# Optimization experiments

Measured on AMD Instinct MI355X. Metric: run time of the kernel, lower is better.

The kernel has to match this reference:

```python
import jax, jax.numpy as jnp
import numpy as np
from jax import lax

K = 3  # kernel size
CO = 64  # out_channels
CI = 64  # in_channels


def setup_inputs() -> dict:
    key = jax.random.key(0)
    k1, k2, k3, k4, k5 = jax.random.split(key, 5)
    x = jax.random.normal(k1, (16, CI, 128, 128), dtype=jnp.float32)
    w1 = jax.random.normal(k2, (2 * CI, 32), dtype=jnp.float32) * 0.05
    b1 = jax.random.normal(k3, (32,), dtype=jnp.float32) * 0.05
    w2 = jax.random.normal(k4, (32, CO * CI * K * K), dtype=jnp.float32) * 0.05
    b2 = jax.random.normal(k5, (CO * CI * K * K,), dtype=jnp.float32) * 0.05
    return {"x": x, "w1": w1, "b1": b1, "w2": w2, "b2": b2}


def reference(x, w1, b1, w2, b2):
    B = x.shape[0]
    # per-sample channel statistics over spatial dims (torch.std is unbiased, ddof=1)
    mean = jnp.mean(x, axis=(2, 3))                      # [B, CI]
    std = jnp.std(x, axis=(2, 3), ddof=1)                # [B, CI]
    stats = jnp.concatenate([mean, std], axis=-1)        # [B, 2*CI]
    h = jax.nn.relu(stats @ w1 + b1)                     # [B, 32]
    kernels = (h @ w2 + b2).reshape(B, CO, CI, K, K)     # per-sample conv kernels

    def conv_one(xi, wi):
        # xi: [CI,H,W], wi: [CO,CI,K,K]; stride=1, padding=1, no bias
        return lax.conv_general_dilated(
            xi[None], wi, window_strides=(1, 1), padding=[(1, 1), (1, 1)],
            dimension_numbers=("NCHW", "OIHW", "NCHW"))[0]

    return jax.vmap(conv_one)(x, kernels)                # [B, CO, H, W]
```

## Files before the change

### kernel.cpp

```cpp
#include <hip/hip_runtime.h>
#include <hip/hip_bf16.h>


#define B_ 16
#define NPIX 16384
#define KEL 36864
#define XT_RS 8320

typedef __attribute__((ext_vector_type(4))) float f32x4;
typedef __attribute__((ext_vector_type(8))) short short8;

static __device__ __forceinline__ short bf16_of(float f) {
    __hip_bfloat16 h = __float2bfloat16(f);
    return *reinterpret_cast<short*>(&h);
}

__global__ __launch_bounds__(256) void xpose_stats(const float* __restrict__ x,
                                                   short* __restrict__ xT,
                                                   float* __restrict__ part) {
    int b = blockIdx.x, cig = blockIdx.y, pt = blockIdx.z;
    int t = threadIdx.x;
    int y = pt * 8 + (t >> 5);
    int x0 = (t & 31) * 4;

    const float* xb = x + ((size_t)(b * 64 + cig * 8)) * NPIX;
    short* xTb = xT + (size_t)b * 128 * XT_RS;

    float s[8], ss[8];
    f32x4 v[8];
    #pragma unroll
    for (int c = 0; c < 8; c++) {
        v[c] = *(const f32x4*)(xb + (size_t)c * NPIX + y * 128 + x0);
        s[c]  = v[c][0] + v[c][1] + v[c][2] + v[c][3];
        ss[c] = v[c][0]*v[c][0] + v[c][1]*v[c][1] + v[c][2]*v[c][2] + v[c][3]*v[c][3];
    }
    #pragma unroll
    for (int xi = 0; xi < 4; xi++) {
        short8 o;
        #pragma unroll
        for (int c = 0; c < 8; c++) o[c] = bf16_of(v[c][xi]);
        *(short8*)(xTb + ((size_t)(y * 130 + x0 + xi + 1)) * 64 + cig * 8) = o;
    }
    if (t < 16) {
        int y2 = pt * 8 + (t & 7);
        int col = (t & 8) ? 129 : 0;
        short8 z = {0, 0, 0, 0, 0, 0, 0, 0};
        *(short8*)(xTb + ((size_t)(y2 * 130 + col)) * 64 + cig * 8) = z;
    }

    __shared__ float red[4][16];
    int lane = t & 63, w = t >> 6;
    #pragma unroll
    for (int c = 0; c < 8; c++) {
        float a = s[c], q = ss[c];
        for (int off = 32; off; off >>= 1) { a += __shfl_down(a, off); q += __shfl_down(q, off); }
        if (lane == 0) { red[w][c * 2] = a; red[w][c * 2 + 1] = q; }
    }
    __syncthreads();
    if (t < 16)
        part[((size_t)((b * 8 + cig) * 16 + pt)) * 16 + t] =
            red[0][t] + red[1][t] + red[2][t] + red[3][t];
}

__global__ __launch_bounds__(256) void kern_gen(const float* __restrict__ part,
                                                const float* __restrict__ w1,
                                                const float* __restrict__ b1,
                                                const float* __restrict__ w2,
                                                const float* __restrict__ b2,
                                                short* __restrict__ wT) {
    __shared__ float st[16][128];
    __shared__ float hT[32][16];
    int t = threadIdx.x;

    for (int id = t; id < 1024; id += 256) {
        int b = id >> 6, ci = id & 63;
        const float* pb = part + ((size_t)((b * 8 + (ci >> 3)) * 16)) * 16 + (ci & 7) * 2;
        float s = 0.f, q = 0.f;
        #pragma unroll
        for (int p = 0; p < 16; p++) { s += pb[p * 16]; q += pb[p * 16 + 1]; }
        float mean = s * (1.f / NPIX);
        float var = fmaxf((q - s * mean) * (1.f / (NPIX - 1)), 0.f);
        st[b][ci] = mean;
        st[b][64 + ci] = sqrtf(var);
    }
    __syncthreads();
    for (int id = t; id < 512; id += 256) {
        int b = id >> 5, jj = id & 31;
        float acc = b1[jj];
        for (int i = 0; i < 128; i++) acc += st[b][i] * w1[i * 32 + jj];
        hT[jj][b] = fmaxf(acc, 0.f);
    }
    __syncthreads();

    int j = blockIdx.x * 128 + (t & 127);
    int bh = t >> 7;
    float wv[32];
    #pragma unroll
    for (int i = 0; i < 32; i++) wv[i] = w2[(size_t)i * KEL + j];
    float bv = b2[j];

    float acc[8];
    #pragma unroll
    for (int k = 0; k < 8; k++) acc[k] = bv;
    #pragma unroll
    for (int i = 0; i < 32; i++) {
        float wvi = wv[i];
        const f32x4* hr = (const f32x4*)&hT[i][bh * 8];
        #pragma unroll
        for (int q4 = 0; q4 < 2; q4++) {
            f32x4 hq = hr[q4];
            acc[q4 * 4 + 0] += hq[0] * wvi;
            acc[q4 * 4 + 1] += hq[1] * wvi;
            acc[q4 * 4 + 2] += hq[2] * wvi;
            acc[q4 * 4 + 3] += hq[3] * wvi;
        }
    }

    int co = j / 576;
    int rem = j - co * 576;
    int ci = rem / 9;
    int tap = rem - ci * 9;
    size_t dst = (size_t)tap * 4096 + co * 64 + ((((ci >> 3) ^ (co & 7)) << 3) | (ci & 7));
    #pragma unroll
    for (int k = 0; k < 8; k++)
        wT[(size_t)(bh * 8 + k) * KEL + dst] = bf16_of(acc[k]);
}

__global__ __launch_bounds__(256, 2) void conv_mfma(const short* __restrict__ xT,
                                                    const short* __restrict__ wT,
                                                    float* __restrict__ out) {
    __shared__ __align__(16) short xls[10 * 272 * 8];
    __shared__ __align__(16) short wls[9 * 256 * 8];

    int b = blockIdx.x;
    int xt = blockIdx.y & 3, cog = blockIdx.y >> 2;
    int ys = blockIdx.z;
    int x0 = xt * 32, y0 = ys * 8;
    int t = threadIdx.x;
    int l = t & 63, w = t >> 6;
    int xq = w & 1, rh = w >> 1;
    int l15 = l & 15, lg = l >> 4;

    const short* xTb = xT + (size_t)b * 128 * XT_RS;
    const short* wTb = wT + (size_t)b * KEL + cog * 2048;

    #pragma unroll
    for (int it = 0; it < 9; it++) {
        __builtin_amdgcn_global_load_lds(
            (const __attribute__((address_space(1))) void*)(wTb + (size_t)it * 4096 + t * 8),
            (__attribute__((address_space(3))) void*)(wls + (it * 256 + (t & ~63)) * 8),
            16, 0, 0);
    }
    #pragma unroll
    for (int lr = 0; lr < 10; lr++) {
        int y = y0 - 1 + lr;
        if (y < 0 || y > 127) {
            short8 z8 = {0, 0, 0, 0, 0, 0, 0, 0};
            #pragma unroll
            for (int it = 0; it < 2; it++) {
                int e = it * 256 + t;
                if (e < 272) *(short8*)(xls + (lr * 272 + e) * 8) = z8;
            }
        } else {
            #pragma unroll
            for (int it = 0; it < 2; it++) {
                int e = it * 256 + t;
                if (e < 272) {
                    int xi = e >> 3, s = e & 7;
                    const short* src = xTb + (size_t)y * XT_RS
                        + (x0 + xi) * 64 + ((s ^ (xi & 7)) << 3);
                    __builtin_amdgcn_global_load_lds(
                        (const __attribute__((address_space(1))) void*)src,
                        (__attribute__((address_space(3))) void*)
                            (xls + (lr * 272 + it * 256 + (t & ~63)) * 8),
                        16, 0, 0);
                }
            }
        }
    }
    asm volatile("s_waitcnt vmcnt(0)" ::: "memory");
    __syncthreads();

    f32x4 acc[2][4];
    #pragma unroll
    for (int f = 0; f < 2; f++)
        #pragma unroll
        for (int r = 0; r < 4; r++) acc[f][r] = (f32x4){0.f, 0.f, 0.f, 0.f};

    #pragma unroll
    for (int kp = 0; kp < 2; kp++) {
        int sig = kp * 4 + lg;
        int pa = sig ^ (l15 & 7);
        #pragma unroll
        for (int tap = 0; tap < 9; tap++) {
            const int dy = tap / 3, dx = tap % 3;
            short8 a0 = *(const short8*)&wls[(tap * 256 + l15 * 8 + pa) * 8];
            short8 a1 = *(const short8*)&wls[(tap * 256 + (16 + l15) * 8 + pa) * 8];
            int xi = xq * 16 + l15 + dx;
            int sw = sig ^ (xi & 7);
            #pragma unroll
            for (int r = 0; r < 4; r++) {
                int row = rh * 4 + r + dy;
                short8 bf = *(const short8*)&xls[(row * 272 + xi * 8 + sw) * 8];
                acc[0][r] = __builtin_amdgcn_mfma_f32_16x16x32_bf16(a0, bf, acc[0][r], 0, 0, 0);
                acc[1][r] = __builtin_amdgcn_mfma_f32_16x16x32_bf16(a1, bf, acc[1][r], 0, 0, 0);
            }
        }
    }

    #pragma unroll
    for (int f = 0; f < 2; f++) {
        #pragma unroll
        for (int reg = 0; reg < 4; reg++) {
            float* ob = out + ((size_t)(b * 64 + cog * 32 + f * 16 + lg * 4 + reg)) * NPIX
                            + (y0 + rh * 4) * 128 + x0 + xq * 16 + l15;
            #pragma unroll
            for (int r = 0; r < 4; r++)
                ob[r * 128] = acc[f][r][reg];
        }
    }
}

extern "C" void kernel_launch(void* const* d_in, const int* in_sizes, int n_in,
                              void* d_out, int out_size, void* d_ws, size_t ws_size,
                              hipStream_t stream) {
    const float* x  = (const float*)d_in[0];
    const float* w1 = (const float*)d_in[1];
    const float* b1 = (const float*)d_in[2];
    const float* w2 = (const float*)d_in[3];
    const float* b2 = (const float*)d_in[4];
    float* out = (float*)d_out;

    float* part = (float*)d_ws;
    short* wT = (short*)((char*)d_ws + 131072);
    short* xT = (short*)((char*)d_ws + 131072 + 1179648);

    xpose_stats<<<dim3(B_, 8, 16), 256, 0, stream>>>(x, xT, part);
    kern_gen<<<dim3(288), 256, 0, stream>>>(part, w1, b1, w2, b2, wT);
    conv_mfma<<<dim3(B_, 8, 16), 256, 0, stream>>>(xT, wT, out);
}
```

Measured before the change: 65.82 us.

## Fuse bf16 transpose of input into conv kernel, drop intermediate xT buffer

The stats kernel no longer writes a padded channel-last bf16 copy of x. The conv kernel now loads fp32 x directly, converts it to bf16, applies padding and writes the swizzled layout into LDS. This removes a large intermediate write and read round trip. The cost is more L2 read bytes, because each of the 8 output-channel groups re-reads fp32 inputs, and the loads become scalar and strided instead of async global-to-LDS copies.

```diff
diff --git a/kernel.cpp b/kernel.cpp
--- a/kernel.cpp
+++ b/kernel.cpp
@@ -5,7 +5,6 @@
 #define B_ 16
 #define NPIX 16384
 #define KEL 36864
-#define XT_RS 8320
 
 typedef __attribute__((ext_vector_type(4))) float f32x4;
 typedef __attribute__((ext_vector_type(8))) short short8;
@@ -15,37 +14,20 @@
     return *reinterpret_cast<short*>(&h);
 }
 
-__global__ __launch_bounds__(256) void xpose_stats(const float* __restrict__ x,
-                                                   short* __restrict__ xT,
-                                                   float* __restrict__ part) {
+__global__ __launch_bounds__(256) void stats_k(const float* __restrict__ x,
+                                               float* __restrict__ part) {
     int b = blockIdx.x, cig = blockIdx.y, pt = blockIdx.z;
     int t = threadIdx.x;
     int y = pt * 8 + (t >> 5);
     int x0 = (t & 31) * 4;
 
     const float* xb = x + ((size_t)(b * 64 + cig * 8)) * NPIX;
-    short* xTb = xT + (size_t)b * 128 * XT_RS;
-
     float s[8], ss[8];
-    f32x4 v[8];
     #pragma unroll
     for (int c = 0; c < 8; c++) {
-        v[c] = *(const f32x4*)(xb + (size_t)c * NPIX + y * 128 + x0);
-        s[c]  = v[c][0] + v[c][1] + v[c][2] + v[c][3];
-        ss[c] = v[c][0]*v[c][0] + v[c][1]*v[c][1] + v[c][2]*v[c][2] + v[c][3]*v[c][3];
-    }
-    #pragma unroll
-    for (int xi = 0; xi < 4; xi++) {
-        short8 o;
-        #pragma unroll
-        for (int c = 0; c < 8; c++) o[c] = bf16_of(v[c][xi]);
-        *(short8*)(xTb + ((size_t)(y * 130 + x0 + xi + 1)) * 64 + cig * 8) = o;
-    }
-    if (t < 16) {
-        int y2 = pt * 8 + (t & 7);
-        int col = (t & 8) ? 129 : 0;
-        short8 z = {0, 0, 0, 0, 0, 0, 0, 0};
-        *(short8*)(xTb + ((size_t)(y2 * 130 + col)) * 64 + cig * 8) = z;
+        f32x4 v = *(const f32x4*)(xb + (size_t)c * NPIX + y * 128 + x0);
+        s[c]  = v[0] + v[1] + v[2] + v[3];
+        ss[c] = v[0]*v[0] + v[1]*v[1] + v[2]*v[2] + v[3]*v[3];
     }
 
     __shared__ float red[4][16];
@@ -126,7 +108,7 @@
         wT[(size_t)(bh * 8 + k) * KEL + dst] = bf16_of(acc[k]);
 }
 
-__global__ __launch_bounds__(256, 2) void conv_mfma(const short* __restrict__ xT,
+__global__ __launch_bounds__(256, 2) void conv_mfma(const float* __restrict__ x,
                                                     const short* __restrict__ wT,
                                                     float* __restrict__ out) {
     __shared__ __align__(16) short xls[10 * 272 * 8];
@@ -141,7 +123,7 @@
     int xq = w & 1, rh = w >> 1;
     int l15 = l & 15, lg = l >> 4;
 
-    const short* xTb = xT + (size_t)b * 128 * XT_RS;
+    const float* xb = x + ((size_t)b * 64) * NPIX;
     const short* wTb = wT + (size_t)b * KEL + cog * 2048;
 
     #pragma unroll
@@ -151,31 +133,24 @@
             (__attribute__((address_space(3))) void*)(wls + (it * 256 + (t & ~63)) * 8),
             16, 0, 0);
     }
-    #pragma unroll
-    for (int lr = 0; lr < 10; lr++) {
-        int y = y0 - 1 + lr;
-        if (y < 0 || y > 127) {
-            short8 z8 = {0, 0, 0, 0, 0, 0, 0, 0};
-            #pragma unroll
-            for (int it = 0; it < 2; it++) {
-                int e = it * 256 + t;
-                if (e < 272) *(short8*)(xls + (lr * 272 + e) * 8) = z8;
+
+    #pragma unroll
+    for (int it = 0; it < 11; it++) {
+        int e = it * 256 + t;
+        if (e < 2720) {
+            int lr = e / 272;
+            int rem = e - lr * 272;
+            int cig = rem / 34;
+            int xi = rem - cig * 34;
+            int y = y0 - 1 + lr;
+            int gx = x0 - 1 + xi;
+            short8 o = {0, 0, 0, 0, 0, 0, 0, 0};
+            if ((unsigned)y < 128u && (unsigned)gx < 128u) {
+                const float* p = xb + (size_t)(cig * 8) * NPIX + y * 128 + gx;
+                #pragma unroll
+                for (int c = 0; c < 8; c++) o[c] = bf16_of(p[(size_t)c * NPIX]);
             }
-        } else {
-            #pragma unroll
-            for (int it = 0; it < 2; it++) {
-                int e = it * 256 + t;
-                if (e < 272) {
-                    int xi = e >> 3, s = e & 7;
-                    const short* src = xTb + (size_t)y * XT_RS
-                        + (x0 + xi) * 64 + ((s ^ (xi & 7)) << 3);
-                    __builtin_amdgcn_global_load_lds(
-                        (const __attribute__((address_space(1))) void*)src,
-                        (__attribute__((address_space(3))) void*)
-                            (xls + (lr * 272 + it * 256 + (t & ~63)) * 8),
-                        16, 0, 0);
-                }
-            }
+            *(short8*)&xls[(lr * 272 + xi * 8 + (cig ^ (xi & 7))) * 8] = o;
         }
     }
     asm volatile("s_waitcnt vmcnt(0)" ::: "memory");
@@ -233,9 +208,8 @@
 
     float* part = (float*)d_ws;
     short* wT = (short*)((char*)d_ws + 131072);
-    short* xT = (short*)((char*)d_ws + 131072 + 1179648);
-
-    xpose_stats<<<dim3(B_, 8, 16), 256, 0, stream>>>(x, xT, part);
+
+    stats_k<<<dim3(B_, 8, 16), 256, 0, stream>>>(x, part);
     kern_gen<<<dim3(288), 256, 0, stream>>>(part, w1, b1, w2, b2, wT);
-    conv_mfma<<<dim3(B_, 8, 16), 256, 0, stream>>>(xT, wT, out);
-}
+    conv_mfma<<<dim3(B_, 8, 16), 256, 0, stream>>>(x, wT, out);
+}
```

Measured after the change: 69.34 us. 1.05x slower.
